# Kernel tuning notes

Measured on AMD Instinct MI355X. Metric: run time of the kernel, lower is better.

The kernel has to match this reference:

```python
import jax, jax.numpy as jnp
import numpy as np

N_HEAD = 8
HID = 256
V_DIM = HID // N_HEAD
NQ = 2048
NK = 2048
BATCH = 16
LOCALITY = 50.0  # percentile threshold; <=100 enables local masking


def setup_inputs() -> dict:
    key = jax.random.key(0)
    k1, k2, k3, k4 = jax.random.split(key, 4)
    m_dist = jax.random.uniform(k1, (N_HEAD, NQ, NK), dtype=jnp.float32)
    x = jax.random.normal(k2, (BATCH, NK, HID), dtype=jnp.float32)
    r = jax.random.normal(k3, (N_HEAD, 1, 1), dtype=jnp.float32)
    weight = jax.random.normal(k4, (N_HEAD, HID, V_DIM), dtype=jnp.float32) / jnp.sqrt(
        jnp.float32(HID)
    )
    return {"m_dist": m_dist, "x": x, "r": r, "weight": weight}


def reference(m_dist, x, r, weight):
    # distance scaling: tan(pi/4 * (1-eps) * (1 + sin(r))), per head
    scale = jnp.tan(0.25 * jnp.pi * (1.0 - 1e-07) * (1.0 + jnp.sin(r)))  # [H,1,1]
    scaled = m_dist * scale  # [H, Nq, Nk]
    # percentile-threshold local masking per (head, query) row
    thr = jnp.percentile(scaled, LOCALITY, axis=-1, keepdims=True)  # [H, Nq, 1]
    scaled = jnp.where(scaled <= thr, scaled, jnp.inf)
    att = jax.nn.softmax(-scaled, axis=-1)  # [H, Nq, Nk]
    value = jnp.einsum("bnj,hjk->bhnk", x, weight)  # [B, H, Nk, v]
    out = jnp.einsum("hjn,bhnk->bhjk", att, value)  # [B, H, Nq, v]
    out = jnp.transpose(out, (0, 2, 1, 3)).reshape(out.shape[0], out.shape[2], -1)
    return jax.nn.gelu(out)  # [B, Nq, HID]
```

## Files before the change

### kernel.cpp

```cpp
#include <hip/hip_runtime.h>
#include <hip/hip_bf16.h>

#define NH   8
#define HID  256
#define VD   32
#define NQ   2048
#define NKK  2048
#define NB   16
#define NN   512

typedef short bf16x8 __attribute__((ext_vector_type(8)));
typedef float f32x4 __attribute__((ext_vector_type(4)));

__device__ inline unsigned short f2bf(float f) {
  unsigned int u = __float_as_uint(f);
  u += 0x7FFFu + ((u >> 16) & 1u);
  return (unsigned short)(u >> 16);
}

__device__ inline void gload_lds16(const void* g, void* l) {
  __builtin_amdgcn_global_load_lds(
      (const __attribute__((address_space(1))) void*)g,
      (__attribute__((address_space(3))) void*)l, 16, 0, 0);
}

__device__ inline float gelu_f(float x) {
  float x3 = x * x * x;
  float u = 0.7978845608028654f * (x + 0.044715f * x3);
  float th = tanhf(u);
  return 0.5f * x * (1.0f + th);
}

__global__ __launch_bounds__(256) void wt_kernel(
    const float* __restrict__ w, unsigned short* __restrict__ wT) {
  const int n = blockIdx.x;
  const int j = threadIdx.x;
  wT[(size_t)n * HID + j] = f2bf(w[(size_t)(n >> 5) * HID * VD + (size_t)j * VD + (n & 31)]);
}

__global__ __launch_bounds__(256) void value_kernel(
    const unsigned short* __restrict__ wT, const float* __restrict__ x,
    unsigned short* __restrict__ vT) {
  const int hvt = blockIdx.x & 1;
  const int kt  = blockIdx.x >> 1;
  const int b   = blockIdx.y;
  const int m0 = hvt * 128;
  const int n0 = kt * 128;
  const int t = threadIdx.x;
  const int lane = t & 63, wid = t >> 6;
  const int wr = wid >> 1, wc = wid & 1;

  __shared__ __align__(16) unsigned short As[128 * 32];
  __shared__ __align__(16) unsigned short Bs[128 * 32];

  const int rowL = t >> 2, cb = (t & 3) * 8;
  const unsigned short* gA0 = wT + (size_t)(m0 + rowL) * HID + cb;
  const unsigned short* gA1 = gA0 + (size_t)64 * HID;
  char* lA0 = (char*)As + t * 16;
  char* lA1 = (char*)As + 4096 + t * 16;

  const int brow = t >> 1, bj = (t & 1) * 16;
  const float* gB = x + ((size_t)b * NKK + n0 + brow) * HID + bj;
  unsigned short* lB = Bs + brow * 32 + bj;

  f32x4 acc[4][4];
#pragma unroll
  for (int i = 0; i < 4; ++i)
#pragma unroll
    for (int j = 0; j < 4; ++j) acc[i][j] = (f32x4){0.f, 0.f, 0.f, 0.f};

  const int fr = lane & 15;
  const int kb = (lane >> 4) * 16;
  const char* baseA = (const char*)As + (wr * 64 + fr) * 64 + kb;
  const char* baseB = (const char*)Bs + (wc * 64 + fr) * 64 + kb;

  f32x4 p0 = *(const f32x4*)(gB + 0);
  f32x4 p1 = *(const f32x4*)(gB + 4);
  f32x4 p2 = *(const f32x4*)(gB + 8);
  f32x4 p3 = *(const f32x4*)(gB + 12);

  for (int kk = 0; kk < HID / 32; ++kk) {
    gload_lds16(gA0, lA0);
    gload_lds16(gA1, lA1);
    gA0 += 32; gA1 += 32;

    f32x4 c0 = p0, c1 = p1, c2 = p2, c3 = p3;
    if (kk < HID / 32 - 1) {
      const float* nb = gB + (kk + 1) * 32;
      p0 = *(const f32x4*)(nb + 0);
      p1 = *(const f32x4*)(nb + 4);
      p2 = *(const f32x4*)(nb + 8);
      p3 = *(const f32x4*)(nb + 12);
    }
    uint4 pk0, pk1;
    pk0.x = (unsigned)f2bf(c0[0]) | ((unsigned)f2bf(c0[1]) << 16);
    pk0.y = (unsigned)f2bf(c0[2]) | ((unsigned)f2bf(c0[3]) << 16);
    pk0.z = (unsigned)f2bf(c1[0]) | ((unsigned)f2bf(c1[1]) << 16);
    pk0.w = (unsigned)f2bf(c1[2]) | ((unsigned)f2bf(c1[3]) << 16);
    pk1.x = (unsigned)f2bf(c2[0]) | ((unsigned)f2bf(c2[1]) << 16);
    pk1.y = (unsigned)f2bf(c2[2]) | ((unsigned)f2bf(c2[3]) << 16);
    pk1.z = (unsigned)f2bf(c3[0]) | ((unsigned)f2bf(c3[1]) << 16);
    pk1.w = (unsigned)f2bf(c3[2]) | ((unsigned)f2bf(c3[3]) << 16);
    *(uint4*)lB = pk0;
    *(uint4*)(lB + 8) = pk1;

    __syncthreads();

    bf16x8 a[4], bfr[4];
#pragma unroll
    for (int i = 0; i < 4; ++i) a[i] = *(const bf16x8*)(baseA + i * 16 * 64);
#pragma unroll
    for (int j = 0; j < 4; ++j) bfr[j] = *(const bf16x8*)(baseB + j * 16 * 64);
#pragma unroll
    for (int i = 0; i < 4; ++i)
#pragma unroll
      for (int j = 0; j < 4; ++j)
        acc[i][j] = __builtin_amdgcn_mfma_f32_16x16x32_bf16(a[i], bfr[j], acc[i][j], 0, 0, 0);
    __syncthreads();
  }

  const int hvb = m0 + wr * 64 + (lane >> 4) * 4;
  const int kc0 = n0 + wc * 64 + (lane & 15);
#pragma unroll
  for (int i = 0; i < 4; ++i) {
#pragma unroll
    for (int j = 0; j < 4; ++j) {
      int kc = kc0 + j * 16;
#pragma unroll
      for (int e = 0; e < 4; ++e) {
        int hv = hvb + i * 16 + e;
        int h = hv >> 5, v = hv & 31;
        vT[((size_t)h * NN + b * VD + v) * NKK + kc] = f2bf(acc[i][j][e]);
      }
    }
  }
}

__global__ __launch_bounds__(256) void att_kernel(
    const float* __restrict__ m_dist, const float* __restrict__ r,
    unsigned short* __restrict__ att) {
  const int row = blockIdx.x;
  const int h = row >> 11;
  const int t = threadIdx.x;
  const int wid = t >> 6;
  const float* md = m_dist + (size_t)row * NKK;

  __shared__ unsigned int hist[256];
  __shared__ float coll[160];
  __shared__ unsigned int collCnt;
  __shared__ int sBA, sBB;
  __shared__ unsigned int sBelow;
  __shared__ unsigned int wtot[4];
  __shared__ float wmin[4], wsumsh[4];
  __shared__ float sVa, sVb;

  float rr = r[h];
  const float C = (float)(0.25 * 3.141592653589793 * (1.0 - 1e-7));
  float sc = tanf(C * (1.0f + sinf(rr)));

  hist[t] = 0u;
  if (t == 0) collCnt = 0u;
  __syncthreads();

  float m[8];
#pragma unroll
  for (int j = 0; j < 8; ++j) m[j] = md[t + 256 * j];

  float mn = m[0];
#pragma unroll
  for (int j = 1; j < 8; ++j) mn = fminf(mn, m[j]);
#pragma unroll
  for (int j = 0; j < 8; ++j) {
    int bin = (int)(m[j] * 256.0f);
    bin = min(max(bin, 0), 255);
    atomicAdd(&hist[bin], 1u);
  }
#pragma unroll
  for (int off = 32; off > 0; off >>= 1) mn = fminf(mn, __shfl_down(mn, off));
  if ((t & 63) == 0) wmin[wid] = mn;
  __syncthreads();

  unsigned int c = hist[t];
  unsigned int xs2 = c;
  for (int off = 1; off < 64; off <<= 1) {
    unsigned int y = __shfl_up(xs2, off);
    if ((t & 63) >= off) xs2 += y;
  }
  if ((t & 63) == 63) wtot[wid] = xs2;
  __syncthreads();
  unsigned int base = 0;
  for (int wq = 0; wq < 4; ++wq)
    if (wq < wid) base += wtot[wq];
  unsigned int cum = xs2 + base;
  if (cum >= 1024u && cum - c < 1024u) { sBA = t; sBelow = cum - c; }
  if (cum >= 1025u && cum - c < 1025u) { sBB = t; }
  __syncthreads();

  const int bA = sBA, bB = sBB;
  const unsigned int below = sBelow;
#pragma unroll
  for (int j = 0; j < 8; ++j) {
    int bin = (int)(m[j] * 256.0f);
    bin = min(max(bin, 0), 255);
    if (bin >= bA && bin <= bB) {
      unsigned int idx = atomicAdd(&collCnt, 1u);
      if (idx < 160u) coll[idx] = m[j];
    }
  }
  __syncthreads();
  const int n = (int)min(collCnt, 160u);
  const int ra = 1023 - (int)below, rb = 1024 - (int)below;
  if (t < n) {
    float v = coll[t];
    int rank = 0;
    for (int j2 = 0; j2 < n; ++j2) {
      float u = coll[j2];
      rank += (u < v || (u == v && j2 < t)) ? 1 : 0;
    }
    if (rank == ra) sVa = v;
    if (rank == rb) sVb = v;
  }
  __syncthreads();

  float mtot = fminf(fminf(wmin[0], wmin[1]), fminf(wmin[2], wmin[3]));
  float minscaled = mtot * sc;
  float ap = sVa * sc, bp = sVb * sc;
  float thr = 0.5f * ap + 0.5f * bp;

  float wv[8];
  float wsum = 0.f;
#pragma unroll
  for (int j = 0; j < 8; ++j) {
    float s = m[j] * sc;
    float e = (s <= thr) ? __expf(minscaled - s) : 0.f;
    wv[j] = e;
    wsum += e;
  }
#pragma unroll
  for (int off = 32; off > 0; off >>= 1) wsum += __shfl_down(wsum, off);
  if ((t & 63) == 0) wsumsh[wid] = wsum;
  __syncthreads();
  float denom = wsumsh[0] + wsumsh[1] + wsumsh[2] + wsumsh[3];
  float inv = 1.0f / denom;

  unsigned short* ao = att + (size_t)row * NKK;
#pragma unroll
  for (int j = 0; j < 8; ++j) ao[t + 256 * j] = f2bf(wv[j] * inv);
}

__global__ __launch_bounds__(256) void gemm_kernel(
    const unsigned short* __restrict__ att, const unsigned short* __restrict__ vT,
    float* __restrict__ out) {
  const int bid = blockIdx.x;
  const int h = bid & 7;
  const int tile = bid >> 3;
  const int qt = tile >> 2, nt = tile & 3;
  const int q0 = qt * 128, n0 = nt * 128;
  const int t = threadIdx.x;
  const int lane = t & 63, wid = t >> 6;
  const int wr = wid >> 1, wc = wid & 1;

  __shared__ __align__(16) unsigned short As[128 * 32];
  __shared__ __align__(16) unsigned short Bs[128 * 32];

  const int rowL = t >> 2;
  const int cb = (t & 3) * 8;

  const unsigned short* gA0 = att + ((size_t)h * NQ + q0 + rowL) * NKK + cb;
  const unsigned short* gA1 = gA0 + (size_t)64 * NKK;
  const unsigned short* gB0 = vT + ((size_t)h * NN + n0 + rowL) * NKK + cb;
  const unsigned short* gB1 = gB0 + (size_t)64 * NKK;

  char* lA0 = (char*)As + t * 16;
  char* lA1 = (char*)As + 4096 + t * 16;
  char* lB0 = (char*)Bs + t * 16;
  char* lB1 = (char*)Bs + 4096 + t * 16;

  f32x4 acc[4][4];
#pragma unroll
  for (int i = 0; i < 4; ++i)
#pragma unroll
    for (int j = 0; j < 4; ++j) acc[i][j] = (f32x4){0.f, 0.f, 0.f, 0.f};

  const int fr = lane & 15;
  const int kb = (lane >> 4) * 16;
  const char* baseA = (const char*)As + (wr * 64 + fr) * 64 + kb;
  const char* baseB = (const char*)Bs + (wc * 64 + fr) * 64 + kb;

  for (int kt = 0; kt < NKK / 32; ++kt) {
    gload_lds16(gA0, lA0);
    gload_lds16(gA1, lA1);
    gload_lds16(gB0, lB0);
    gload_lds16(gB1, lB1);
    gA0 += 32; gA1 += 32; gB0 += 32; gB1 += 32;
    __syncthreads();

    bf16x8 a[4], b[4];
#pragma unroll
    for (int i = 0; i < 4; ++i) a[i] = *(const bf16x8*)(baseA + i * 16 * 64);
#pragma unroll
    for (int j = 0; j < 4; ++j) b[j] = *(const bf16x8*)(baseB + j * 16 * 64);
#pragma unroll
    for (int i = 0; i < 4; ++i)
#pragma unroll
      for (int j = 0; j < 4; ++j)
        acc[i][j] = __builtin_amdgcn_mfma_f32_16x16x32_bf16(a[i], b[j], acc[i][j], 0, 0, 0);
    __syncthreads();
  }

  const int orow = q0 + wr * 64 + (lane >> 4) * 4;
  const int ocol0 = n0 + wc * 64 + (lane & 15);
#pragma unroll
  for (int i = 0; i < 4; ++i) {
#pragma unroll
    for (int j = 0; j < 4; ++j) {
      int ncol = ocol0 + j * 16;
      int bb = ncol >> 5, vv = ncol & 31;
      float* op = out + ((size_t)bb * NQ + orow + i * 16) * HID + h * VD + vv;
#pragma unroll
      for (int e = 0; e < 4; ++e) op[(size_t)e * HID] = gelu_f(acc[i][j][e]);
    }
  }
}

extern "C" void kernel_launch(void* const* d_in, const int* in_sizes, int n_in,
                              void* d_out, int out_size, void* d_ws, size_t ws_size,
                              hipStream_t stream) {
  const float* m_dist = (const float*)d_in[0];
  const float* x      = (const float*)d_in[1];
  const float* r      = (const float*)d_in[2];
  const float* weight = (const float*)d_in[3];
  float* out = (float*)d_out;

  unsigned short* att = (unsigned short*)d_ws;
  unsigned short* vT  = (unsigned short*)((char*)d_ws + (size_t)NH * NQ * NKK * 2);
  unsigned short* wT  = (unsigned short*)((char*)d_ws + (size_t)NH * NQ * NKK * 2 +
                                          (size_t)NH * NN * NKK * 2);

  wt_kernel<<<dim3(256), dim3(256), 0, stream>>>(weight, wT);
  value_kernel<<<dim3(32, NB), dim3(256), 0, stream>>>(wT, x, vT);
  att_kernel<<<dim3(NH * NQ), dim3(256), 0, stream>>>(m_dist, r, att);
  gemm_kernel<<<dim3(NH * 64), dim3(256), 0, stream>>>(att, vT, out);
}
```

Before: 114.9 us.

## Pipeline GEMM k-loop with 4-stage LDS ring and cheaper GELU

The attention-times-value GEMM kernel now uses a four-buffer LDS ring. It prefetches three k-tiles ahead with async global-to-LDS loads and waits on partial vmcnt plus a single barrier per step, where before every iteration had two full syncs and an exposed load latency. The GELU epilogue also swaps tanhf for an exp-based tanh formula. The risks are LDS usage rising to 64KB, which may limit occupancy, and a race from the ring reuse: the loads for the next stage are issued after fragments are read but before other waves finish their reads. The exp form can also overflow to inf/inf (NaN) for large inputs.

```diff
diff --git a/kernel.cpp b/kernel.cpp
--- a/kernel.cpp
+++ b/kernel.cpp
@@ -25,10 +25,9 @@
 }
 
 __device__ inline float gelu_f(float x) {
-  float x3 = x * x * x;
-  float u = 0.7978845608028654f * (x + 0.044715f * x3);
-  float th = tanhf(u);
-  return 0.5f * x * (1.0f + th);
+  float u2 = 1.5957691216057308f * (x + 0.044715f * x * x * x);
+  float e = __expf(u2);
+  return 0.5f * x * (1.0f + (e - 1.0f) / (e + 1.0f));
 }
 
 __global__ __launch_bounds__(256) void wt_kernel(
@@ -260,21 +259,26 @@
   const int lane = t & 63, wid = t >> 6;
   const int wr = wid >> 1, wc = wid & 1;
 
-  __shared__ __align__(16) unsigned short As[128 * 32];
-  __shared__ __align__(16) unsigned short Bs[128 * 32];
+  __shared__ __align__(16) unsigned short As[4][128 * 32];
+  __shared__ __align__(16) unsigned short Bs[4][128 * 32];
 
   const int rowL = t >> 2;
   const int cb = (t & 3) * 8;
 
-  const unsigned short* gA0 = att + ((size_t)h * NQ + q0 + rowL) * NKK + cb;
-  const unsigned short* gA1 = gA0 + (size_t)64 * NKK;
-  const unsigned short* gB0 = vT + ((size_t)h * NN + n0 + rowL) * NKK + cb;
-  const unsigned short* gB1 = gB0 + (size_t)64 * NKK;
-
-  char* lA0 = (char*)As + t * 16;
-  char* lA1 = (char*)As + 4096 + t * 16;
-  char* lB0 = (char*)Bs + t * 16;
-  char* lB1 = (char*)Bs + 4096 + t * 16;
+  const unsigned short* gA = att + ((size_t)h * NQ + q0 + rowL) * NKK + cb;
+  const unsigned short* gB = vT + ((size_t)h * NN + n0 + rowL) * NKK + cb;
+  const int ldsOff = t * 16;
+
+#define STAGE(BI, KT) do {                                                  \
+    const unsigned short* a_ = gA + (KT) * 32;                              \
+    const unsigned short* b_ = gB + (KT) * 32;                              \
+    char* lA_ = (char*)As[(BI)] + ldsOff;                                   \
+    char* lB_ = (char*)Bs[(BI)] + ldsOff;                                   \
+    gload_lds16(a_, lA_);                                                   \
+    gload_lds16(a_ + (size_t)64 * NKK, lA_ + 4096);                         \
+    gload_lds16(b_, lB_);                                                   \
+    gload_lds16(b_ + (size_t)64 * NKK, lB_ + 4096);                         \
+  } while (0)
 
   f32x4 acc[4][4];
 #pragma unroll
@@ -284,29 +288,35 @@
 
   const int fr = lane & 15;
   const int kb = (lane >> 4) * 16;
-  const char* baseA = (const char*)As + (wr * 64 + fr) * 64 + kb;
-  const char* baseB = (const char*)Bs + (wc * 64 + fr) * 64 + kb;
-
-  for (int kt = 0; kt < NKK / 32; ++kt) {
-    gload_lds16(gA0, lA0);
-    gload_lds16(gA1, lA1);
-    gload_lds16(gB0, lB0);
-    gload_lds16(gB1, lB1);
-    gA0 += 32; gA1 += 32; gB0 += 32; gB1 += 32;
-    __syncthreads();
-
-    bf16x8 a[4], b[4];
-#pragma unroll
-    for (int i = 0; i < 4; ++i) a[i] = *(const bf16x8*)(baseA + i * 16 * 64);
-#pragma unroll
-    for (int j = 0; j < 4; ++j) b[j] = *(const bf16x8*)(baseB + j * 16 * 64);
-#pragma unroll
-    for (int i = 0; i < 4; ++i)
-#pragma unroll
-      for (int j = 0; j < 4; ++j)
-        acc[i][j] = __builtin_amdgcn_mfma_f32_16x16x32_bf16(a[i], b[j], acc[i][j], 0, 0, 0);
-    __syncthreads();
-  }
+  const int fragOff = (wr * 64 + fr) * 64 + kb;
+  const int fragOffB = (wc * 64 + fr) * 64 + kb;
+
+  STAGE(0, 0);
+  STAGE(1, 1);
+  STAGE(2, 2);
+  asm volatile("s_waitcnt vmcnt(8)\n\ts_barrier" ::: "memory");
+
+  for (int kt = 0; kt < 64; kt += 4) {
+#pragma unroll
+    for (int u = 0; u < 4; ++u) {
+      const char* bA = (const char*)As[u] + fragOff;
+      const char* bB = (const char*)Bs[u] + fragOffB;
+      bf16x8 a[4], b[4];
+#pragma unroll
+      for (int i = 0; i < 4; ++i) a[i] = *(const bf16x8*)(bA + i * 1024);
+#pragma unroll
+      for (int j = 0; j < 4; ++j) b[j] = *(const bf16x8*)(bB + j * 1024);
+      STAGE((u + 3) & 3, (kt + u + 3) & 63);
+#pragma unroll
+      for (int i = 0; i < 4; ++i)
+#pragma unroll
+        for (int j = 0; j < 4; ++j)
+          acc[i][j] = __builtin_amdgcn_mfma_f32_16x16x32_bf16(a[i], b[j], acc[i][j], 0, 0, 0);
+      asm volatile("s_waitcnt vmcnt(8)\n\ts_barrier" ::: "memory");
+    }
+  }
+  asm volatile("s_waitcnt vmcnt(0)" ::: "memory");
+#undef STAGE
 
   const int orow = q0 + wr * 64 + (lane >> 4) * 4;
   const int ocol0 = n0 + wc * 64 + (lane & 15);
```

Measured after the change: 113.0 us. No clear change (-1.6%).
